# Optimization experiments

Measured on AMD Instinct MI355X. Metric: run time of the kernel, lower is better.

The kernel has to match this reference:

```python
import jax, jax.numpy as jnp
import numpy as np

EPS = 1e-12  # matches torch F.normalize eps


def _l2_normalize(x, axis=-1):
    # torch.F.normalize: x / max(||x||, eps)
    n = jnp.sqrt(jnp.sum(x * x, axis=axis, keepdims=True))
    return x / jnp.maximum(n, EPS)


def setup_inputs() -> dict:
    N, n_classes, embed_dim = 32768, 1000, 1024
    key = jax.random.key(0)
    k_feat, k_lab, k_proto = jax.random.split(key, 3)

    features = jax.random.normal(k_feat, (N, embed_dim), dtype=jnp.float32)

    # one-hot float labels, as expected by `torch.matmul(labels, self.mean_class)`
    y = jax.random.randint(k_lab, (N,), 0, n_classes)
    labels = jax.nn.one_hot(y, n_classes, dtype=jnp.float32)

    # predefined prototypes: orthonormal rows (ortho_group.rvs equivalent via QR)
    g = jax.random.normal(k_proto, (embed_dim, embed_dim), dtype=jnp.float32)
    q, _ = jnp.linalg.qr(g)
    mean_class = q[:n_classes]  # [n_classes, embed_dim], orthonormal rows

    return {"features": features, "labels": labels, "mean_class": mean_class}


def reference(features, labels, mean_class):
    # features: [N, D]; labels: [N, C] one-hot; mean_class: [C, D]
    # (3-D feature mean-pooling branch not exercised: inputs are 2-D)
    proto_y = labels @ mean_class                 # [N, D]
    f = _l2_normalize(features, axis=1)
    p = _l2_normalize(proto_y, axis=1)
    # diag(f @ p.T) == rowwise dot product -> same math, O(N*D) not O(N^2*D)
    cos = jnp.einsum("nd,nd->n", f, p)            # [N]
    return jnp.mean(1.0 - cos)
```

## Files before the change

### kernel.cpp

```cpp
#include <hip/hip_runtime.h>

constexpr int N_CLASSES = 1000;
constexpr int EMBED     = 1024;

typedef float floatx4 __attribute__((ext_vector_type(4)));

__device__ __forceinline__ floatx4 ntload(const floatx4* p) {
    return __builtin_nontemporal_load(p);
}

__global__ __launch_bounds__(256, 4) void angular_pipelined_kernel(
    const float* __restrict__ features,
    const float* __restrict__ labels,
    const float* __restrict__ mean_class,
    float* __restrict__ partials,
    int n_rows)
{
    const int tid  = threadIdx.x;
    const int lane = tid & 63;
    const int wave = tid >> 6;
    const int wave_id = (blockIdx.x * blockDim.x + tid) >> 6;
    const int n_waves = (gridDim.x * blockDim.x) >> 6;

    const float wb = (float)(4 * lane + 1);
    const floatx4 w0 = {wb,          wb + 1.f,        wb + 2.f,        wb + 3.f};
    const floatx4 w1 = {wb + 256.f,  wb + 257.f,      wb + 258.f,      wb + 259.f};
    const floatx4 w2 = {wb + 512.f,  wb + 513.f,      wb + 514.f,      wb + 515.f};
    const floatx4 w3 = {wb + 768.f,  wb + 769.f,      wb + 770.f,      wb + 771.f};

    float acc = 0.0f;

    floatx4 af0, af1, af2, af3, al0, al1, al2, al3;
    floatx4 bf0, bf1, bf2, bf3, bl0, bl1, bl2, bl3;

    #define LOAD_ROW(F0, F1, F2, F3, L0, L1, L2, L3, ROW) do {                     \
        const floatx4* frow_ = (const floatx4*)(features + (size_t)(ROW) * EMBED); \
        F0 = ntload(frow_ + lane);        F1 = ntload(frow_ + lane + 64);          \
        F2 = ntload(frow_ + lane + 128);  F3 = ntload(frow_ + lane + 192);         \
        const floatx4* lrow_ = (const floatx4*)(labels + (size_t)(ROW) * N_CLASSES); \
        L0 = ntload(lrow_ + lane);        L1 = ntload(lrow_ + lane + 64);          \
        L2 = ntload(lrow_ + lane + 128);                                           \
        L3 = (lane < N_CLASSES / 4 - 192) ? ntload(lrow_ + lane + 192)             \
                                          : (floatx4){0.f, 0.f, 0.f, 0.f};         \
    } while (0)

    #define CONSUME_ROW(F0, F1, F2, F3, L0, L1, L2, L3) do {                       \
                        \
        float candf = L0.x*w0.x + L0.y*w0.y + L0.z*w0.z + L0.w*w0.w;               \
        candf += L1.x*w1.x + L1.y*w1.y + L1.z*w1.z + L1.w*w1.w;                    \
        candf += L2.x*w2.x + L2.y*w2.y + L2.z*w2.z + L2.w*w2.w;                    \
        candf += L3.x*w3.x + L3.y*w3.y + L3.z*w3.z + L3.w*w3.w;                    \
        unsigned long long m_ = __ballot(candf != 0.0f);                           \
        float clsf = __shfl(candf, __ffsll(m_) - 1, 64);                           \
        int cls = (int)clsf - 1;                                                   \
        cls = __builtin_amdgcn_readfirstlane(cls);                                 \
        const floatx4* prow_ = (const floatx4*)(mean_class + (size_t)cls * EMBED); \
        floatx4 p0 = prow_[lane];                                                  \
        floatx4 p1 = prow_[lane + 64];                                             \
        floatx4 p2 = prow_[lane + 128];                                            \
        floatx4 p3 = prow_[lane + 192];                                            \
        float ff = 0.f, pp = 0.f, fp = 0.f;                                        \
        ff += F0.x*F0.x + F0.y*F0.y + F0.z*F0.z + F0.w*F0.w;                       \
        pp += p0.x*p0.x + p0.y*p0.y + p0.z*p0.z + p0.w*p0.w;                       \
        fp += F0.x*p0.x + F0.y*p0.y + F0.z*p0.z + F0.w*p0.w;                       \
        ff += F1.x*F1.x + F1.y*F1.y + F1.z*F1.z + F1.w*F1.w;                       \
        pp += p1.x*p1.x + p1.y*p1.y + p1.z*p1.z + p1.w*p1.w;                       \
        fp += F1.x*p1.x + F1.y*p1.y + F1.z*p1.z + F1.w*p1.w;                       \
        ff += F2.x*F2.x + F2.y*F2.y + F2.z*F2.z + F2.w*F2.w;                       \
        pp += p2.x*p2.x + p2.y*p2.y + p2.z*p2.z + p2.w*p2.w;                       \
        fp += F2.x*p2.x + F2.y*p2.y + F2.z*p2.z + F2.w*p2.w;                       \
        ff += F3.x*F3.x + F3.y*F3.y + F3.z*F3.z + F3.w*F3.w;                       \
        pp += p3.x*p3.x + p3.y*p3.y + p3.z*p3.z + p3.w*p3.w;                       \
        fp += F3.x*p3.x + F3.y*p3.y + F3.z*p3.z + F3.w*p3.w;                       \
        _Pragma("unroll")                                                          \
        for (int msk_ = 1; msk_ < 64; msk_ <<= 1) {                                \
            ff += __shfl_xor(ff, msk_, 64);                                        \
            pp += __shfl_xor(pp, msk_, 64);                                        \
            fp += __shfl_xor(fp, msk_, 64);                                        \
        }                                                                          \
        acc += 1.0f - fp * __builtin_amdgcn_rsqf(fmaxf(ff * pp, 1e-24f));          \
    } while (0)

    int r = wave_id;
    if (r < n_rows) LOAD_ROW(af0, af1, af2, af3, al0, al1, al2, al3, r);

    while (r < n_rows) {
        int rn = r + n_waves;
        if (rn < n_rows) LOAD_ROW(bf0, bf1, bf2, bf3, bl0, bl1, bl2, bl3, rn);
        CONSUME_ROW(af0, af1, af2, af3, al0, al1, al2, al3);
        r = rn;
        if (r >= n_rows) break;

        rn = r + n_waves;
        if (rn < n_rows) LOAD_ROW(af0, af1, af2, af3, al0, al1, al2, al3, rn);
        CONSUME_ROW(bf0, bf1, bf2, bf3, bl0, bl1, bl2, bl3);
        r = rn;
    }

    #undef LOAD_ROW
    #undef CONSUME_ROW

    __shared__ float s_red[4];
    if (lane == 0) s_red[wave] = acc;
    __syncthreads();
    if (tid == 0)
        partials[blockIdx.x] = s_red[0] + s_red[1] + s_red[2] + s_red[3];
}

__global__ __launch_bounds__(256) void reduce_partials_kernel(
    const float* __restrict__ partials, int num_partials,
    float* __restrict__ out, float inv_n)
{
    const int tid  = threadIdx.x;
    const int lane = tid & 63;
    const int wave = tid >> 6;
    __shared__ float s_red[4];

    float acc = 0.0f;
    for (int i = tid; i < num_partials; i += 256)
        acc += partials[i];
    #pragma unroll
    for (int msk = 1; msk < 64; msk <<= 1)
        acc += __shfl_xor(acc, msk, 64);
    if (lane == 0) s_red[wave] = acc;
    __syncthreads();
    if (tid == 0)
        out[0] = (s_red[0] + s_red[1] + s_red[2] + s_red[3]) * inv_n;
}

extern "C" void kernel_launch(void* const* d_in, const int* in_sizes, int n_in,
                              void* d_out, int out_size, void* d_ws, size_t ws_size,
                              hipStream_t stream) {
    const float* features   = (const float*)d_in[0];
    const float* labels     = (const float*)d_in[1];
    const float* mean_class = (const float*)d_in[2];
    float* out = (float*)d_out;
    float* partials = (float*)d_ws;

    const int n_rows = in_sizes[0] / EMBED;
    const int num_blocks = 1024;

    angular_pipelined_kernel<<<num_blocks, 256, 0, stream>>>(
        features, labels, mean_class, partials, n_rows);
    reduce_partials_kernel<<<1, 256, 0, stream>>>(
        partials, num_blocks, out, 1.0f / (float)n_rows);
}
```

Measured before the change: 267.0 us.

## Split label scan and feature dot into separate kernels with precomputed class norms

Splits the fused kernel into a class-norm precompute, a label-scan kernel that writes a per-row (class, norm²) record, and a feature-dot kernel. The dot kernel now knows each row's class before its loads, so the prototype row load can be issued together with the feature load instead of waiting on the label reduction. It also drops the per-row prototype norm computation and its wave reduction. The cost is two extra launches and a small record buffer written and then read back. Both kernels still stream the same total bytes of labels and features.

```diff
diff --git a/kernel.cpp b/kernel.cpp
--- a/kernel.cpp
+++ b/kernel.cpp
@@ -5,16 +5,96 @@
 
 typedef float floatx4 __attribute__((ext_vector_type(4)));
 
+struct RowRec { int cls; float pp; };
+
 __device__ __forceinline__ floatx4 ntload(const floatx4* p) {
     return __builtin_nontemporal_load(p);
 }
 
-__global__ __launch_bounds__(256, 4) void angular_pipelined_kernel(
+__global__ __launch_bounds__(256) void class_norm_kernel(
+    const float* __restrict__ mean_class, float* __restrict__ pp_out)
+{
+    const int tid  = threadIdx.x;
+    const int lane = tid & 63;
+    const int wid  = (blockIdx.x * blockDim.x + tid) >> 6;
+    if (wid >= N_CLASSES) return;
+    const floatx4* prow = (const floatx4*)(mean_class + (size_t)wid * EMBED);
+    floatx4 p0 = prow[lane];
+    floatx4 p1 = prow[lane + 64];
+    floatx4 p2 = prow[lane + 128];
+    floatx4 p3 = prow[lane + 192];
+    float pp = 0.f;
+    pp += p0.x*p0.x + p0.y*p0.y + p0.z*p0.z + p0.w*p0.w;
+    pp += p1.x*p1.x + p1.y*p1.y + p1.z*p1.z + p1.w*p1.w;
+    pp += p2.x*p2.x + p2.y*p2.y + p2.z*p2.z + p2.w*p2.w;
+    pp += p3.x*p3.x + p3.y*p3.y + p3.z*p3.z + p3.w*p3.w;
+    #pragma unroll
+    for (int m = 1; m < 64; m <<= 1) pp += __shfl_xor(pp, m, 64);
+    if (lane == 0) pp_out[wid] = pp;
+}
+
+__global__ __launch_bounds__(256, 4) void label_scan_kernel(
+    const float* __restrict__ labels,
+    const float* __restrict__ pp_arr,
+    RowRec* __restrict__ rec, int n_rows)
+{
+    const int tid  = threadIdx.x;
+    const int lane = tid & 63;
+    const int wave_id = (blockIdx.x * blockDim.x + tid) >> 6;
+    const int n_waves = (gridDim.x * blockDim.x) >> 6;
+
+    const float wb = (float)(4 * lane + 1);
+    const floatx4 w0 = {wb,          wb + 1.f,   wb + 2.f,   wb + 3.f};
+    const floatx4 w1 = {wb + 256.f,  wb + 257.f, wb + 258.f, wb + 259.f};
+    const floatx4 w2 = {wb + 512.f,  wb + 513.f, wb + 514.f, wb + 515.f};
+    const floatx4 w3 = {wb + 768.f,  wb + 769.f, wb + 770.f, wb + 771.f};
+
+    floatx4 a0, a1, a2, a3, b0, b1, b2, b3;
+
+    #define LOADL(L0, L1, L2, L3, ROW) do {                                        \
+        const floatx4* lr_ = (const floatx4*)(labels + (size_t)(ROW) * N_CLASSES); \
+        L0 = ntload(lr_ + lane);       L1 = ntload(lr_ + lane + 64);               \
+        L2 = ntload(lr_ + lane + 128);                                             \
+        L3 = (lane < N_CLASSES / 4 - 192) ? ntload(lr_ + lane + 192)               \
+                                          : (floatx4){0.f, 0.f, 0.f, 0.f};         \
+    } while (0)
+
+    #define SCANROW(L0, L1, L2, L3, ROW) do {                                      \
+        float c_ = L0.x*w0.x + L0.y*w0.y + L0.z*w0.z + L0.w*w0.w;                  \
+        c_ += L1.x*w1.x + L1.y*w1.y + L1.z*w1.z + L1.w*w1.w;                       \
+        c_ += L2.x*w2.x + L2.y*w2.y + L2.z*w2.z + L2.w*w2.w;                       \
+        c_ += L3.x*w3.x + L3.y*w3.y + L3.z*w3.z + L3.w*w3.w;                       \
+        unsigned long long m_ = __ballot(c_ != 0.0f);                              \
+        float cf_ = __shfl(c_, __ffsll(m_) - 1, 64);                               \
+        int cls_ = (int)cf_ - 1;                                                   \
+        if (lane == 0) {                                                           \
+            RowRec rr_; rr_.cls = cls_; rr_.pp = pp_arr[cls_];                     \
+            rec[ROW] = rr_;                                                        \
+        }                                                                          \
+    } while (0)
+
+    int r = wave_id;
+    if (r < n_rows) LOADL(a0, a1, a2, a3, r);
+    while (r < n_rows) {
+        int rn = r + n_waves;
+        if (rn < n_rows) LOADL(b0, b1, b2, b3, rn);
+        SCANROW(a0, a1, a2, a3, r);
+        r = rn;
+        if (r >= n_rows) break;
+        rn = r + n_waves;
+        if (rn < n_rows) LOADL(a0, a1, a2, a3, rn);
+        SCANROW(b0, b1, b2, b3, r);
+        r = rn;
+    }
+    #undef LOADL
+    #undef SCANROW
+}
+
+__global__ __launch_bounds__(256, 4) void feature_dot_kernel(
     const float* __restrict__ features,
-    const float* __restrict__ labels,
     const float* __restrict__ mean_class,
-    float* __restrict__ partials,
-    int n_rows)
+    const RowRec* __restrict__ rec,
+    float* __restrict__ partials, int n_rows)
 {
     const int tid  = threadIdx.x;
     const int lane = tid & 63;
@@ -22,83 +102,79 @@
     const int wave_id = (blockIdx.x * blockDim.x + tid) >> 6;
     const int n_waves = (gridDim.x * blockDim.x) >> 6;
 
-    const float wb = (float)(4 * lane + 1);
-    const floatx4 w0 = {wb,          wb + 1.f,        wb + 2.f,        wb + 3.f};
-    const floatx4 w1 = {wb + 256.f,  wb + 257.f,      wb + 258.f,      wb + 259.f};
-    const floatx4 w2 = {wb + 512.f,  wb + 513.f,      wb + 514.f,      wb + 515.f};
-    const floatx4 w3 = {wb + 768.f,  wb + 769.f,      wb + 770.f,      wb + 771.f};
-
     float acc = 0.0f;
 
-    floatx4 af0, af1, af2, af3, al0, al1, al2, al3;
-    floatx4 bf0, bf1, bf2, bf3, bl0, bl1, bl2, bl3;
-
-    #define LOAD_ROW(F0, F1, F2, F3, L0, L1, L2, L3, ROW) do {                     \
-        const floatx4* frow_ = (const floatx4*)(features + (size_t)(ROW) * EMBED); \
-        F0 = ntload(frow_ + lane);        F1 = ntload(frow_ + lane + 64);          \
-        F2 = ntload(frow_ + lane + 128);  F3 = ntload(frow_ + lane + 192);         \
-        const floatx4* lrow_ = (const floatx4*)(labels + (size_t)(ROW) * N_CLASSES); \
-        L0 = ntload(lrow_ + lane);        L1 = ntload(lrow_ + lane + 64);          \
-        L2 = ntload(lrow_ + lane + 128);                                           \
-        L3 = (lane < N_CLASSES / 4 - 192) ? ntload(lrow_ + lane + 192)             \
-                                          : (floatx4){0.f, 0.f, 0.f, 0.f};         \
-    } while (0)
-
-    #define CONSUME_ROW(F0, F1, F2, F3, L0, L1, L2, L3) do {                       \
-                        \
-        float candf = L0.x*w0.x + L0.y*w0.y + L0.z*w0.z + L0.w*w0.w;               \
-        candf += L1.x*w1.x + L1.y*w1.y + L1.z*w1.z + L1.w*w1.w;                    \
-        candf += L2.x*w2.x + L2.y*w2.y + L2.z*w2.z + L2.w*w2.w;                    \
-        candf += L3.x*w3.x + L3.y*w3.y + L3.z*w3.z + L3.w*w3.w;                    \
-        unsigned long long m_ = __ballot(candf != 0.0f);                           \
-        float clsf = __shfl(candf, __ffsll(m_) - 1, 64);                           \
-        int cls = (int)clsf - 1;                                                   \
-        cls = __builtin_amdgcn_readfirstlane(cls);                                 \
-        const floatx4* prow_ = (const floatx4*)(mean_class + (size_t)cls * EMBED); \
-        floatx4 p0 = prow_[lane];                                                  \
-        floatx4 p1 = prow_[lane + 64];                                             \
-        floatx4 p2 = prow_[lane + 128];                                            \
-        floatx4 p3 = prow_[lane + 192];                                            \
-        float ff = 0.f, pp = 0.f, fp = 0.f;                                        \
+    floatx4 fa0, fa1, fa2, fa3, pa0, pa1, pa2, pa3;
+    floatx4 fb0, fb1, fb2, fb3, pb0, pb1, pb2, pb3;
+
+    #define LOADF(F0, F1, F2, F3, ROW) do {                                        \
+        const floatx4* fr_ = (const floatx4*)(features + (size_t)(ROW) * EMBED);   \
+        F0 = ntload(fr_ + lane);       F1 = ntload(fr_ + lane + 64);               \
+        F2 = ntload(fr_ + lane + 128); F3 = ntload(fr_ + lane + 192);              \
+    } while (0)
+
+    #define LOADP(P0, P1, P2, P3, CLS) do {                                        \
+        int c_ = __builtin_amdgcn_readfirstlane(CLS);                              \
+        const floatx4* pr_ = (const floatx4*)(mean_class + (size_t)c_ * EMBED);    \
+        P0 = pr_[lane];       P1 = pr_[lane + 64];                                 \
+        P2 = pr_[lane + 128]; P3 = pr_[lane + 192];                                \
+    } while (0)
+
+    #define CONSUME(F0, F1, F2, F3, P0, P1, P2, P3, PP) do {                       \
+        float ff = 0.f, fp = 0.f;                                                  \
         ff += F0.x*F0.x + F0.y*F0.y + F0.z*F0.z + F0.w*F0.w;                       \
-        pp += p0.x*p0.x + p0.y*p0.y + p0.z*p0.z + p0.w*p0.w;                       \
-        fp += F0.x*p0.x + F0.y*p0.y + F0.z*p0.z + F0.w*p0.w;                       \
+        fp += F0.x*P0.x + F0.y*P0.y + F0.z*P0.z + F0.w*P0.w;                       \
         ff += F1.x*F1.x + F1.y*F1.y + F1.z*F1.z + F1.w*F1.w;                       \
-        pp += p1.x*p1.x + p1.y*p1.y + p1.z*p1.z + p1.w*p1.w;                       \
-        fp += F1.x*p1.x + F1.y*p1.y + F1.z*p1.z + F1.w*p1.w;                       \
+        fp += F1.x*P1.x + F1.y*P1.y + F1.z*P1.z + F1.w*P1.w;                       \
         ff += F2.x*F2.x + F2.y*F2.y + F2.z*F2.z + F2.w*F2.w;                       \
-        pp += p2.x*p2.x + p2.y*p2.y + p2.z*p2.z + p2.w*p2.w;                       \
-        fp += F2.x*p2.x + F2.y*p2.y + F2.z*p2.z + F2.w*p2.w;                       \
+        fp += F2.x*P2.x + F2.y*P2.y + F2.z*P2.z + F2.w*P2.w;                       \
         ff += F3.x*F3.x + F3.y*F3.y + F3.z*F3.z + F3.w*F3.w;                       \
-        pp += p3.x*p3.x + p3.y*p3.y + p3.z*p3.z + p3.w*p3.w;                       \
-        fp += F3.x*p3.x + F3.y*p3.y + F3.z*p3.z + F3.w*p3.w;                       \
+        fp += F3.x*P3.x + F3.y*P3.y + F3.z*P3.z + F3.w*P3.w;                       \
         _Pragma("unroll")                                                          \
-        for (int msk_ = 1; msk_ < 64; msk_ <<= 1) {                                \
-            ff += __shfl_xor(ff, msk_, 64);                                        \
-            pp += __shfl_xor(pp, msk_, 64);                                        \
-            fp += __shfl_xor(fp, msk_, 64);                                        \
+        for (int m_ = 1; m_ < 64; m_ <<= 1) {                                      \
+            ff += __shfl_xor(ff, m_, 64);                                          \
+            fp += __shfl_xor(fp, m_, 64);                                          \
         }                                                                          \
-        acc += 1.0f - fp * __builtin_amdgcn_rsqf(fmaxf(ff * pp, 1e-24f));          \
+        acc += 1.0f - fp * __builtin_amdgcn_rsqf(fmaxf(ff * (PP), 1e-24f));        \
     } while (0)
 
     int r = wave_id;
-    if (r < n_rows) LOAD_ROW(af0, af1, af2, af3, al0, al1, al2, al3, r);
+    RowRec recA, recB, recC;
+    if (r < n_rows) {
+        recA = rec[r];
+        int r1 = r + n_waves;
+        if (r1 < n_rows) recB = rec[r1];
+        LOADF(fa0, fa1, fa2, fa3, r);
+        LOADP(pa0, pa1, pa2, pa3, recA.cls);
+    }
 
     while (r < n_rows) {
         int rn = r + n_waves;
-        if (rn < n_rows) LOAD_ROW(bf0, bf1, bf2, bf3, bl0, bl1, bl2, bl3, rn);
-        CONSUME_ROW(af0, af1, af2, af3, al0, al1, al2, al3);
+        if (rn < n_rows) {
+            LOADF(fb0, fb1, fb2, fb3, rn);
+            LOADP(pb0, pb1, pb2, pb3, recB.cls);
+            int rnn = rn + n_waves;
+            if (rnn < n_rows) recC = rec[rnn];
+        }
+        CONSUME(fa0, fa1, fa2, fa3, pa0, pa1, pa2, pa3, recA.pp);
+        recA = recB; recB = recC;
         r = rn;
         if (r >= n_rows) break;
 
         rn = r + n_waves;
-        if (rn < n_rows) LOAD_ROW(af0, af1, af2, af3, al0, al1, al2, al3, rn);
-        CONSUME_ROW(bf0, bf1, bf2, bf3, bl0, bl1, bl2, bl3);
+        if (rn < n_rows) {
+            LOADF(fa0, fa1, fa2, fa3, rn);
+            LOADP(pa0, pa1, pa2, pa3, recB.cls);
+            int rnn = rn + n_waves;
+            if (rnn < n_rows) recC = rec[rnn];
+        }
+        CONSUME(fb0, fb1, fb2, fb3, pb0, pb1, pb2, pb3, recA.pp);
+        recA = recB; recB = recC;
         r = rn;
     }
-
-    #undef LOAD_ROW
-    #undef CONSUME_ROW
+    #undef LOADF
+    #undef LOADP
+    #undef CONSUME
 
     __shared__ float s_red[4];
     if (lane == 0) s_red[wave] = acc;
@@ -135,13 +211,20 @@
     const float* labels     = (const float*)d_in[1];
     const float* mean_class = (const float*)d_in[2];
     float* out = (float*)d_out;
-    float* partials = (float*)d_ws;
+
+    float*  partials = (float*)d_ws;
+    float*  pp_arr   = (float*)((char*)d_ws + 4096);
+    RowRec* rec      = (RowRec*)((char*)d_ws + 8192);
 
     const int n_rows = in_sizes[0] / EMBED;
     const int num_blocks = 1024;
 
-    angular_pipelined_kernel<<<num_blocks, 256, 0, stream>>>(
-        features, labels, mean_class, partials, n_rows);
+    class_norm_kernel<<<(N_CLASSES * 64 + 255) / 256, 256, 0, stream>>>(
+        mean_class, pp_arr);
+    label_scan_kernel<<<num_blocks, 256, 0, stream>>>(
+        labels, pp_arr, rec, n_rows);
+    feature_dot_kernel<<<num_blocks, 256, 0, stream>>>(
+        features, mean_class, rec, partials, n_rows);
     reduce_partials_kernel<<<1, 256, 0, stream>>>(
         partials, num_blocks, out, 1.0f / (float)n_rows);
 }
```

New measurement: 262.1 us. Within noise of the previous version (-1.8%).
